# Kernel tuning notes

Hardware: AMD Instinct MI355X
Metric: run time of the kernel (lower is better)

The kernel has to match this reference:

```python
import jax, jax.numpy as jnp
import numpy as np

N, F_IN, HID, E, G = 100000, 256, 256, 800000, 256


def setup_inputs() -> dict:
    key = jax.random.key(0)
    ks = jax.random.split(key, 10)
    x = jax.random.normal(ks[0], (N, F_IN), dtype=jnp.float32)
    edge_index = jax.random.randint(ks[1], (2, E), 0, N, dtype=jnp.int64)
    batch = jnp.sort(jax.random.randint(ks[2], (N,), 0, G, dtype=jnp.int64))
    s = 1.0 / np.sqrt(HID)
    W1 = jax.random.normal(ks[3], (F_IN, HID), dtype=jnp.float32) * s
    b1 = jnp.zeros((HID,), dtype=jnp.float32)
    W2 = jax.random.normal(ks[4], (HID, HID), dtype=jnp.float32) * s
    b2 = jnp.zeros((HID,), dtype=jnp.float32)
    Wc1 = jax.random.normal(ks[5], (HID, HID // 2), dtype=jnp.float32) * s
    bc1 = jnp.zeros((HID // 2,), dtype=jnp.float32)
    Wc2 = jax.random.normal(ks[6], (HID // 2, 2), dtype=jnp.float32) * s
    bc2 = jnp.zeros((2,), dtype=jnp.float32)
    return dict(x=x, edge_index=edge_index, batch=batch, num_graphs=G,
                W1=W1, b1=b1, W2=W2, b2=b2, Wc1=Wc1, bc1=bc1, Wc2=Wc2, bc2=bc2)


def _gcn_layer(h, src, dst, inv_sqrt_deg, W, b):
    # GCNConv: D^-1/2 (A + I) D^-1/2 (h W) + b
    hw = h @ W                                            # (N, H)
    coef = inv_sqrt_deg[src] * inv_sqrt_deg[dst]          # (E,)
    msgs = hw[src] * coef[:, None]                        # (E, H)
    agg = jax.ops.segment_sum(msgs, dst, num_segments=h.shape[0])
    self_loop = hw * (inv_sqrt_deg * inv_sqrt_deg)[:, None]
    return agg + self_loop + b


def reference(x, edge_index, batch, num_graphs, W1, b1, W2, b2, Wc1, bc1, Wc2, bc2):
    n = x.shape[0]
    src, dst = edge_index[0], edge_index[1]
    # degree with self-loops (symmetric normalization)
    deg = jax.ops.segment_sum(jnp.ones((src.shape[0],), jnp.float32), dst,
                              num_segments=n) + 1.0
    inv_sqrt_deg = jax.lax.rsqrt(deg)

    h = jax.nn.relu(_gcn_layer(x, src, dst, inv_sqrt_deg, W1, b1))
    node_emb = jax.nn.relu(_gcn_layer(h, src, dst, inv_sqrt_deg, W2, b2))

    # per-graph mean pooling (segment mean replacing the Python loop)
    sums = jax.ops.segment_sum(node_emb, batch, num_segments=num_graphs)
    counts = jax.ops.segment_sum(jnp.ones((n,), jnp.float32), batch,
                                 num_segments=num_graphs)
    graph_emb = sums / jnp.maximum(counts, 1.0)[:, None]

    # classifier MLP (dropout is identity in eval mode)
    hcls = jax.nn.relu(graph_emb @ Wc1 + bc1)
    logits = hcls @ Wc2 + bc2                             # (G, 2)
    return logits, node_emb
```

## Files before the change

kernel.cpp:

```cpp
#include <hip/hip_runtime.h>
#include <hip/hip_bf16.h>

#define HID 256
#define NGRAPH 256

typedef __bf16 bf16_t;
typedef __attribute__((ext_vector_type(8))) __bf16 bf16x8;
typedef __attribute__((ext_vector_type(4))) __bf16 bf16x4;
typedef __attribute__((ext_vector_type(4))) float f32x4;

__global__ void zero_int_kernel(int* __restrict__ p, int n) {
    int i = blockIdx.x * blockDim.x + threadIdx.x;
    if (i < n) p[i] = 0;
}

__global__ void count_deg_kernel(const int* __restrict__ ei, int E, int* __restrict__ deg) {
    int e = blockIdx.x * blockDim.x + threadIdx.x;
    if (e >= E) return;
    int dst = ei[E + e];
    atomicAdd(&deg[dst], 1);
}

#define SCHUNK 512

__global__ __launch_bounds__(256) void scan_pass1_kernel(
    const int* __restrict__ deg, int N, int* __restrict__ bsum) {
    __shared__ int red[256];
    int b = blockIdx.x, t = threadIdx.x;
    int i0 = b * SCHUNK + 2 * t;
    int v = 0;
    if (i0 < N) v += deg[i0];
    if (i0 + 1 < N) v += deg[i0 + 1];
    red[t] = v;
    __syncthreads();
    for (int s = 128; s > 0; s >>= 1) {
        if (t < s) red[t] += red[t + s];
        __syncthreads();
    }
    if (t == 0) bsum[b] = red[0];
}

__global__ __launch_bounds__(256) void scan_pass2_kernel(
    const int* __restrict__ bsum, int NB, int* __restrict__ boff) {
    __shared__ int s[256];
    int t = threadIdx.x;
    int v = (t < NB) ? bsum[t] : 0;
    s[t] = v;
    __syncthreads();
    for (int off = 1; off < 256; off <<= 1) {
        int x = s[t];
        if (t >= off) x += s[t - off];
        __syncthreads();
        s[t] = x;
        __syncthreads();
    }
    if (t < NB) boff[t] = s[t] - v;
}

__global__ __launch_bounds__(256) void scan_pass3_kernel(
    const int* __restrict__ deg, int N, const int* __restrict__ boff,
    int* __restrict__ rowptr, int* __restrict__ cursor, float* __restrict__ invd) {
    __shared__ int s[256];
    int b = blockIdx.x, t = threadIdx.x;
    int i0 = b * SCHUNK + 2 * t;
    int d0 = (i0 < N) ? deg[i0] : 0;
    int d1 = (i0 + 1 < N) ? deg[i0 + 1] : 0;
    int pair = d0 + d1;
    s[t] = pair;
    __syncthreads();
    for (int off = 1; off < 256; off <<= 1) {
        int x = s[t];
        if (t >= off) x += s[t - off];
        __syncthreads();
        s[t] = x;
        __syncthreads();
    }
    int excl = s[t] - pair + boff[b];
    if (i0 < N) {
        rowptr[i0] = excl;
        cursor[i0] = excl;
        invd[i0] = rsqrtf((float)d0 + 1.0f);
    }
    if (i0 + 1 < N) {
        int e1 = excl + d0;
        rowptr[i0 + 1] = e1;
        cursor[i0 + 1] = e1;
        invd[i0 + 1] = rsqrtf((float)d1 + 1.0f);
    }
}

__global__ void fill_csr_kernel(const int* __restrict__ ei, int E,
                                int* __restrict__ cursor, int* __restrict__ csr_src) {
    int e = blockIdx.x * blockDim.x + threadIdx.x;
    if (e >= E) return;
    int src = ei[e];
    int dst = ei[E + e];
    int pos = atomicAdd(&cursor[dst], 1);
    csr_src[pos] = src;
}

__global__ __launch_bounds__(256) void wsplit_kernel(
    const float* __restrict__ W, bf16_t* __restrict__ Wf) {
    int idx = blockIdx.x * 256 + threadIdx.x;
    float w = W[idx];
    int k = idx >> 8, n = idx & 255;
    int k0 = k >> 5, kg = (k >> 3) & 3, j = k & 7;
    int nt = n >> 4, m = n & 15;
    Wf[(size_t)(((k0 * 16 + nt) * 64) + kg * 16 + m) * 8 + j] = (bf16_t)w;
}

#define GBM 64

template <int SPLIT>
__global__ __launch_bounds__(256, 2) void gemm_mfma_kernel(
    const void* __restrict__ Xv, const bf16_t* __restrict__ Wf,
    const float* __restrict__ rowscale, bf16_t* __restrict__ out, int Nrows) {
    __shared__ bf16_t Blds[32768];

    const int tid = threadIdx.x;
    const int wave = tid >> 6;
    const int lane = tid & 63;
    const int row0 = blockIdx.x * GBM;
    const int m = lane & 15;
    const int kg = lane >> 4;

    const int arow_raw = row0 + wave * 16 + m;
    const int arow = (arow_raw < Nrows) ? arow_raw : 0;

    f32x4 acc[16];
#pragma unroll
    for (int i = 0; i < 16; ++i) acc[i] = (f32x4){0.f, 0.f, 0.f, 0.f};

#pragma unroll
    for (int c = 0; c < 2; ++c) {
        float4 xa0, xb0, xa1, xb1, xa2, xb2, xa3, xb3;
        bf16x8 ah0, ah1, ah2, ah3;
        if (SPLIT) {
            const float* xr = (const float*)Xv + (size_t)arow * 256 + c * 128 + kg * 8;
            xa0 = *(const float4*)&xr[0];   xb0 = *(const float4*)&xr[4];
            xa1 = *(const float4*)&xr[32];  xb1 = *(const float4*)&xr[36];
            xa2 = *(const float4*)&xr[64];  xb2 = *(const float4*)&xr[68];
            xa3 = *(const float4*)&xr[96];  xb3 = *(const float4*)&xr[100];
        } else {
            const bf16_t* xr = (const bf16_t*)Xv + (size_t)arow * 256 + c * 128 + kg * 8;
            ah0 = *(const bf16x8*)&xr[0];
            ah1 = *(const bf16x8*)&xr[32];
            ah2 = *(const bf16x8*)&xr[64];
            ah3 = *(const bf16x8*)&xr[96];
        }

        if (c) __syncthreads();
#pragma unroll
        for (int it = 0; it < 16; ++it)
            *(bf16x8*)&Blds[it * 2048 + tid * 8] =
                *(const bf16x8*)&Wf[c * 32768 + it * 2048 + tid * 8];
        __syncthreads();

#pragma unroll
        for (int k0c = 0; k0c < 4; ++k0c) {
            bf16x8 ah, al;
            if (SPLIT) {
                float4 xa = (k0c == 0) ? xa0 : (k0c == 1) ? xa1 : (k0c == 2) ? xa2 : xa3;
                float4 xb = (k0c == 0) ? xb0 : (k0c == 1) ? xb1 : (k0c == 2) ? xb2 : xb3;
                float xf[8] = {xa.x, xa.y, xa.z, xa.w, xb.x, xb.y, xb.z, xb.w};
#pragma unroll
                for (int q = 0; q < 8; ++q) {
                    bf16_t hi = (bf16_t)xf[q];
                    ah[q] = hi;
                    al[q] = (bf16_t)(xf[q] - (float)hi);
                }
            } else {
                ah = (k0c == 0) ? ah0 : (k0c == 1) ? ah1 : (k0c == 2) ? ah2 : ah3;
            }
            bf16x8 bh[16];
#pragma unroll
            for (int nt = 0; nt < 16; ++nt)
                bh[nt] = *(const bf16x8*)&Blds[(k0c * 16 + nt) * 512 + lane * 8];
#pragma unroll
            for (int nt = 0; nt < 16; ++nt) {
                acc[nt] = __builtin_amdgcn_mfma_f32_16x16x32_bf16(ah, bh[nt], acc[nt], 0, 0, 0);
                if (SPLIT)
                    acc[nt] = __builtin_amdgcn_mfma_f32_16x16x32_bf16(al, bh[nt], acc[nt], 0, 0, 0);
            }
        }
    }

    const int rbase = row0 + wave * 16 + kg * 4;
#pragma unroll
    for (int j = 0; j < 4; ++j) {
        int r = rbase + j;
        if (r < Nrows) {
            float sc = rowscale[r];
#pragma unroll
            for (int nt = 0; nt < 16; ++nt)
                out[(size_t)r * 256 + nt * 16 + m] = (bf16_t)(acc[nt][j] * sc);
        }
    }
}

template <typename OutT>
__global__ __launch_bounds__(256) void gcn_aggregate_kernel(
    const bf16_t* __restrict__ hs, const int* __restrict__ rowptr,
    const int* __restrict__ deg, const int* __restrict__ csr_src,
    const float* __restrict__ inv_d, const float* __restrict__ bias,
    OutT* __restrict__ out, int N) {
    int gwid = (blockIdx.x * blockDim.x + threadIdx.x) >> 6;
    int lane = threadIdx.x & 63;
    if (gwid >= N) return;
    int base = rowptr[gwid];
    int len = deg[gwid];
    int c = lane * 4;

    bf16x4 sv = *(const bf16x4*)&hs[(size_t)gwid * 256 + c];
    float ax0 = (float)sv[0], ay0 = (float)sv[1], az0 = (float)sv[2], aw0 = (float)sv[3];
    float ax1 = 0.f, ay1 = 0.f, az1 = 0.f, aw1 = 0.f;
    float ax2 = 0.f, ay2 = 0.f, az2 = 0.f, aw2 = 0.f;
    float ax3 = 0.f, ay3 = 0.f, az3 = 0.f, aw3 = 0.f;
    int i = 0;
    for (; i + 4 <= len; i += 4) {
        int s0 = csr_src[base + i];
        int s1 = csr_src[base + i + 1];
        int s2 = csr_src[base + i + 2];
        int s3 = csr_src[base + i + 3];
        bf16x4 v0 = *(const bf16x4*)&hs[(size_t)s0 * 256 + c];
        bf16x4 v1 = *(const bf16x4*)&hs[(size_t)s1 * 256 + c];
        bf16x4 v2 = *(const bf16x4*)&hs[(size_t)s2 * 256 + c];
        bf16x4 v3 = *(const bf16x4*)&hs[(size_t)s3 * 256 + c];
        ax0 += (float)v0[0]; ay0 += (float)v0[1]; az0 += (float)v0[2]; aw0 += (float)v0[3];
        ax1 += (float)v1[0]; ay1 += (float)v1[1]; az1 += (float)v1[2]; aw1 += (float)v1[3];
        ax2 += (float)v2[0]; ay2 += (float)v2[1]; az2 += (float)v2[2]; aw2 += (float)v2[3];
        ax3 += (float)v3[0]; ay3 += (float)v3[1]; az3 += (float)v3[2]; aw3 += (float)v3[3];
    }
    for (; i < len; ++i) {
        int s = csr_src[base + i];
        bf16x4 v = *(const bf16x4*)&hs[(size_t)s * 256 + c];
        ax0 += (float)v[0]; ay0 += (float)v[1]; az0 += (float)v[2]; aw0 += (float)v[3];
    }
    float ax = (ax0 + ax1) + (ax2 + ax3);
    float ay = (ay0 + ay1) + (ay2 + ay3);
    float az = (az0 + az1) + (az2 + az3);
    float aw = (aw0 + aw1) + (aw2 + aw3);

    float sc = inv_d[gwid];
    float4 bb = *(const float4*)&bias[c];
    float ox = fmaxf(fmaf(ax, sc, bb.x), 0.f);
    float oy = fmaxf(fmaf(ay, sc, bb.y), 0.f);
    float oz = fmaxf(fmaf(az, sc, bb.z), 0.f);
    float ow = fmaxf(fmaf(aw, sc, bb.w), 0.f);
    if constexpr (sizeof(OutT) == 2) {
        bf16x4 o;
        o[0] = (bf16_t)ox; o[1] = (bf16_t)oy; o[2] = (bf16_t)oz; o[3] = (bf16_t)ow;
        *(bf16x4*)&out[(size_t)gwid * 256 + c] = o;
    } else {
        float4 o = {ox, oy, oz, ow};
        *(float4*)&out[(size_t)gwid * 256 + c] = o;
    }
}

__global__ void graph_bounds_kernel(const int* __restrict__ batch, int N, int G,
                                    int* __restrict__ gstart) {
    int i = blockIdx.x * blockDim.x + threadIdx.x;
    if (i > N) return;
    int cur = (i < N) ? batch[i] : G;
    int prev = (i == 0) ? -1 : batch[i - 1];
    for (int g = prev + 1; g <= cur; ++g) gstart[g] = i;
}

__global__ __launch_bounds__(256) void pool_mean_kernel(
    const float* __restrict__ emb, const int* __restrict__ gstart,
    float* __restrict__ gemb) {
    int g = blockIdx.x;
    int j = threadIdx.x;
    int s = gstart[g], e = gstart[g + 1];
    float s0 = 0.f, s1 = 0.f, s2 = 0.f, s3 = 0.f;
    int n = s;
    for (; n + 4 <= e; n += 4) {
        s0 += emb[(size_t)n * 256 + j];
        s1 += emb[(size_t)(n + 1) * 256 + j];
        s2 += emb[(size_t)(n + 2) * 256 + j];
        s3 += emb[(size_t)(n + 3) * 256 + j];
    }
    for (; n < e; ++n) s0 += emb[(size_t)n * 256 + j];
    float sum = (s0 + s1) + (s2 + s3);
    float cnt = fmaxf((float)(e - s), 1.0f);
    gemb[g * 256 + j] = sum / cnt;
}

__global__ __launch_bounds__(128) void cls1_kernel(
    const float* __restrict__ gemb, const float* __restrict__ Wc1,
    const float* __restrict__ bc1, float* __restrict__ hcls) {
    int g = blockIdx.x;
    int j = threadIdx.x;
    float sum = bc1[j];
    for (int k = 0; k < 256; ++k) sum = fmaf(gemb[g * 256 + k], Wc1[k * 128 + j], sum);
    hcls[g * 128 + j] = fmaxf(sum, 0.f);
}

__global__ void cls2_kernel(const float* __restrict__ hcls, const float* __restrict__ Wc2,
                            const float* __restrict__ bc2, float* __restrict__ logits, int G) {
    int idx = blockIdx.x * blockDim.x + threadIdx.x;
    if (idx >= G * 2) return;
    int g = idx >> 1, c = idx & 1;
    float sum = bc2[c];
    for (int k = 0; k < 128; ++k) sum = fmaf(hcls[g * 128 + k], Wc2[k * 2 + c], sum);
    logits[idx] = sum;
}

extern "C" void kernel_launch(void* const* d_in, const int* in_sizes, int n_in,
                              void* d_out, int out_size, void* d_ws, size_t ws_size,
                              hipStream_t stream) {
    const float* x   = (const float*)d_in[0];
    const int*   ei  = (const int*)d_in[1];
    const int*   batch = (const int*)d_in[2];
    const float* W1  = (const float*)d_in[4];
    const float* b1  = (const float*)d_in[5];
    const float* W2  = (const float*)d_in[6];
    const float* b2  = (const float*)d_in[7];
    const float* Wc1 = (const float*)d_in[8];
    const float* bc1 = (const float*)d_in[9];
    const float* Wc2 = (const float*)d_in[10];
    const float* bc2 = (const float*)d_in[11];

    const int N = in_sizes[0] / HID;
    const int E = in_sizes[1] / 2;
    const int G = NGRAPH;

    float* logits   = (float*)d_out;
    float* node_out = (float*)d_out + (size_t)G * 2;

    char* wsb = (char*)d_ws;
    size_t off = 0;
    auto alloc = [&](size_t bytes) -> void* {
        void* p = wsb + off;
        off += (bytes + 255) & ~(size_t)255;
        return p;
    };
    bf16_t* hs     = (bf16_t*)alloc((size_t)N * HID * 2);
    bf16_t* hb     = (bf16_t*)alloc((size_t)N * HID * 2);
    int*    rowptr = (int*)alloc((size_t)N * 4);
    int*    cursor = (int*)alloc((size_t)N * 4);
    int*    degi   = (int*)alloc((size_t)N * 4);
    int*    csr    = (int*)alloc((size_t)E * 4);
    float*  invd   = (float*)alloc((size_t)N * 4);
    int*    gstart = (int*)alloc((size_t)(G + 1) * 4);
    float*  gemb   = (float*)alloc((size_t)G * HID * 4);
    float*  hcls   = (float*)alloc((size_t)G * (HID / 2) * 4);
    int*    bsum   = (int*)alloc(256 * 4);
    int*    boff   = (int*)alloc(256 * 4);
    bf16_t* wf     = (bf16_t*)alloc((size_t)HID * HID * 2);
    (void)ws_size; (void)n_in; (void)out_size;

    const int NB = (N + SCHUNK - 1) / SCHUNK;

    zero_int_kernel<<<(N + 255) / 256, 256, 0, stream>>>(degi, N);
    count_deg_kernel<<<(E + 255) / 256, 256, 0, stream>>>(ei, E, degi);
    scan_pass1_kernel<<<NB, 256, 0, stream>>>(degi, N, bsum);
    scan_pass2_kernel<<<1, 256, 0, stream>>>(bsum, NB, boff);
    scan_pass3_kernel<<<NB, 256, 0, stream>>>(degi, N, boff, rowptr, cursor, invd);
    fill_csr_kernel<<<(E + 255) / 256, 256, 0, stream>>>(ei, E, cursor, csr);

    const int GB = (N + GBM - 1) / GBM;

    wsplit_kernel<<<HID * HID / 256, 256, 0, stream>>>(W1, wf);
    gemm_mfma_kernel<1><<<GB, 256, 0, stream>>>(x, wf, invd, hs, N);
    gcn_aggregate_kernel<bf16_t><<<(N * 64 + 255) / 256, 256, 0, stream>>>(
        hs, rowptr, degi, csr, invd, b1, hb, N);

    wsplit_kernel<<<HID * HID / 256, 256, 0, stream>>>(W2, wf);
    gemm_mfma_kernel<0><<<GB, 256, 0, stream>>>(hb, wf, invd, hs, N);
    gcn_aggregate_kernel<float><<<(N * 64 + 255) / 256, 256, 0, stream>>>(
        hs, rowptr, degi, csr, invd, b2, node_out, N);

    graph_bounds_kernel<<<(N + 1 + 255) / 256, 256, 0, stream>>>(batch, N, G, gstart);
    pool_mean_kernel<<<G, 256, 0, stream>>>(node_out, gstart, gemb);
    cls1_kernel<<<G, 128, 0, stream>>>(gemb, Wc1, bc1, hcls);
    cls2_kernel<<<(G * 2 + 255) / 256, 256, 0, stream>>>(hcls, Wc2, bc2, logits, G);
}
```

Measured before the change: 383.0 us.

## Bucket CSR neighbor lists by source range and widen pooling parallelism

Degree counting and CSR filling now use per-destination sub-buckets keyed by the high bits of the source index, so each row's neighbor list comes out roughly sorted by source. This is meant to improve gather locality in the aggregation kernels, where rows of the transformed features are read by source index. A row-sum kernel rebuilds the plain degree, and per-bucket cursors are produced during the scan. Mean pooling is also split across four column blocks per graph, with four row groups reduced through shared memory, to raise parallelism. The cost is 16x larger degree and cursor arrays, one extra kernel launch, and extra zeroing traffic.

```diff
diff --git a/kernel.cpp b/kernel.cpp
--- a/kernel.cpp
+++ b/kernel.cpp
@@ -3,6 +3,8 @@
 
 #define HID 256
 #define NGRAPH 256
+#define NBKT 16
+#define BSHIFT 13
 
 typedef __bf16 bf16_t;
 typedef __attribute__((ext_vector_type(8))) __bf16 bf16x8;
@@ -14,11 +16,22 @@
     if (i < n) p[i] = 0;
 }
 
-__global__ void count_deg_kernel(const int* __restrict__ ei, int E, int* __restrict__ deg) {
+__global__ void count_deg2_kernel(const int* __restrict__ ei, int E, int* __restrict__ deg2) {
     int e = blockIdx.x * blockDim.x + threadIdx.x;
     if (e >= E) return;
+    int src = ei[e];
     int dst = ei[E + e];
-    atomicAdd(&deg[dst], 1);
+    atomicAdd(&deg2[dst * NBKT + (src >> BSHIFT)], 1);
+}
+
+__global__ __launch_bounds__(256) void rowsum_kernel(
+    const int* __restrict__ deg2, int N, int* __restrict__ deg) {
+    int i = blockIdx.x * blockDim.x + threadIdx.x;
+    if (i >= N) return;
+    int s = 0;
+#pragma unroll
+    for (int b = 0; b < NBKT; ++b) s += deg2[i * NBKT + b];
+    deg[i] = s;
 }
 
 #define SCHUNK 512
@@ -58,8 +71,9 @@
 }
 
 __global__ __launch_bounds__(256) void scan_pass3_kernel(
-    const int* __restrict__ deg, int N, const int* __restrict__ boff,
-    int* __restrict__ rowptr, int* __restrict__ cursor, float* __restrict__ invd) {
+    const int* __restrict__ deg, const int* __restrict__ deg2, int N,
+    const int* __restrict__ boff, int* __restrict__ rowptr,
+    int* __restrict__ cursor2, float* __restrict__ invd) {
     __shared__ int s[256];
     int b = blockIdx.x, t = threadIdx.x;
     int i0 = b * SCHUNK + 2 * t;
@@ -78,24 +92,34 @@
     int excl = s[t] - pair + boff[b];
     if (i0 < N) {
         rowptr[i0] = excl;
-        cursor[i0] = excl;
         invd[i0] = rsqrtf((float)d0 + 1.0f);
+        int run = excl;
+#pragma unroll
+        for (int bk = 0; bk < NBKT; ++bk) {
+            cursor2[i0 * NBKT + bk] = run;
+            run += deg2[i0 * NBKT + bk];
+        }
     }
     if (i0 + 1 < N) {
         int e1 = excl + d0;
         rowptr[i0 + 1] = e1;
-        cursor[i0 + 1] = e1;
         invd[i0 + 1] = rsqrtf((float)d1 + 1.0f);
+        int run = e1;
+#pragma unroll
+        for (int bk = 0; bk < NBKT; ++bk) {
+            cursor2[(i0 + 1) * NBKT + bk] = run;
+            run += deg2[(i0 + 1) * NBKT + bk];
+        }
     }
 }
 
 __global__ void fill_csr_kernel(const int* __restrict__ ei, int E,
-                                int* __restrict__ cursor, int* __restrict__ csr_src) {
+                                int* __restrict__ cursor2, int* __restrict__ csr_src) {
     int e = blockIdx.x * blockDim.x + threadIdx.x;
     if (e >= E) return;
     int src = ei[e];
     int dst = ei[E + e];
-    int pos = atomicAdd(&cursor[dst], 1);
+    int pos = atomicAdd(&cursor2[dst * NBKT + (src >> BSHIFT)], 1);
     csr_src[pos] = src;
 }
 
@@ -269,21 +293,21 @@
 __global__ __launch_bounds__(256) void pool_mean_kernel(
     const float* __restrict__ emb, const int* __restrict__ gstart,
     float* __restrict__ gemb) {
+    __shared__ float red[4][64];
     int g = blockIdx.x;
-    int j = threadIdx.x;
+    int col = blockIdx.y * 64 + (threadIdx.x & 63);
+    int rg = threadIdx.x >> 6;
     int s = gstart[g], e = gstart[g + 1];
-    float s0 = 0.f, s1 = 0.f, s2 = 0.f, s3 = 0.f;
-    int n = s;
-    for (; n + 4 <= e; n += 4) {
-        s0 += emb[(size_t)n * 256 + j];
-        s1 += emb[(size_t)(n + 1) * 256 + j];
-        s2 += emb[(size_t)(n + 2) * 256 + j];
-        s3 += emb[(size_t)(n + 3) * 256 + j];
-    }
-    for (; n < e; ++n) s0 += emb[(size_t)n * 256 + j];
-    float sum = (s0 + s1) + (s2 + s3);
-    float cnt = fmaxf((float)(e - s), 1.0f);
-    gemb[g * 256 + j] = sum / cnt;
+    float sum = 0.f;
+    for (int n = s + rg; n < e; n += 4) sum += emb[(size_t)n * 256 + col];
+    red[rg][threadIdx.x & 63] = sum;
+    __syncthreads();
+    if (rg == 0) {
+        int l = threadIdx.x & 63;
+        float t = (red[0][l] + red[1][l]) + (red[2][l] + red[3][l]);
+        float cnt = fmaxf((float)(e - s), 1.0f);
+        gemb[g * 256 + col] = t / cnt;
+    }
 }
 
 __global__ __launch_bounds__(128) void cls1_kernel(
@@ -338,7 +362,8 @@
     bf16_t* hs     = (bf16_t*)alloc((size_t)N * HID * 2);
     bf16_t* hb     = (bf16_t*)alloc((size_t)N * HID * 2);
     int*    rowptr = (int*)alloc((size_t)N * 4);
-    int*    cursor = (int*)alloc((size_t)N * 4);
+    int*    deg2   = (int*)alloc((size_t)N * NBKT * 4);
+    int*    cursor2= (int*)alloc((size_t)N * NBKT * 4);
     int*    degi   = (int*)alloc((size_t)N * 4);
     int*    csr    = (int*)alloc((size_t)E * 4);
     float*  invd   = (float*)alloc((size_t)N * 4);
@@ -352,12 +377,13 @@
 
     const int NB = (N + SCHUNK - 1) / SCHUNK;
 
-    zero_int_kernel<<<(N + 255) / 256, 256, 0, stream>>>(degi, N);
-    count_deg_kernel<<<(E + 255) / 256, 256, 0, stream>>>(ei, E, degi);
+    zero_int_kernel<<<(N * NBKT + 255) / 256, 256, 0, stream>>>(deg2, N * NBKT);
+    count_deg2_kernel<<<(E + 255) / 256, 256, 0, stream>>>(ei, E, deg2);
+    rowsum_kernel<<<(N + 255) / 256, 256, 0, stream>>>(deg2, N, degi);
     scan_pass1_kernel<<<NB, 256, 0, stream>>>(degi, N, bsum);
     scan_pass2_kernel<<<1, 256, 0, stream>>>(bsum, NB, boff);
-    scan_pass3_kernel<<<NB, 256, 0, stream>>>(degi, N, boff, rowptr, cursor, invd);
-    fill_csr_kernel<<<(E + 255) / 256, 256, 0, stream>>>(ei, E, cursor, csr);
+    scan_pass3_kernel<<<NB, 256, 0, stream>>>(degi, deg2, N, boff, rowptr, cursor2, invd);
+    fill_csr_kernel<<<(E + 255) / 256, 256, 0, stream>>>(ei, E, cursor2, csr);
 
     const int GB = (N + GBM - 1) / GBM;
 
@@ -372,7 +398,7 @@
         hs, rowptr, degi, csr, invd, b2, node_out, N);
 
     graph_bounds_kernel<<<(N + 1 + 255) / 256, 256, 0, stream>>>(batch, N, G, gstart);
-    pool_mean_kernel<<<G, 256, 0, stream>>>(node_out, gstart, gemb);
+    pool_mean_kernel<<<dim3(G, 4), 256, 0, stream>>>(node_out, gstart, gemb);
     cls1_kernel<<<G, 128, 0, stream>>>(gemb, Wc1, bc1, hcls);
     cls2_kernel<<<(G * 2 + 255) / 256, 256, 0, stream>>>(hcls, Wc2, bc2, logits, G);
 }
```

After: 395.5 us. 3.3% more time.
